# Optimization experiments

Hardware: AMD Instinct MI355X
Metric: run time of the kernel (lower is better)

Reference implementation:

```python
import jax, jax.numpy as jnp
import numpy as np

NUM_USR = 8192
H = 256  # NUM_SOURCE == H (feature dim of y_a); NUM_TARGET = 256


def setup_inputs() -> dict:
    key = jax.random.key(0)
    k1, k2, k3, k4 = jax.random.split(key, 4)
    return {
        "y_a": jax.random.normal(k1, (NUM_USR, H), dtype=jnp.float32),
        "y_b": jax.random.normal(k2, (NUM_USR, H), dtype=jnp.float32),
        "W": jax.random.normal(k3, (H, H), dtype=jnp.float32) * (1.0 / np.sqrt(H)),
        "b": jax.random.normal(k4, (H,), dtype=jnp.float32) * 0.01,
    }


def reference(y_a, y_b, W, b):
    # Linear: proj[j] = W @ y_b[j] + b   (torch nn.Linear convention)
    proj = jnp.einsum("jt,st->js", y_b, W) + b          # [num_usr, H]
    # torch loop computes score[i, j] = y_a[i] . proj[j], replicated H times
    # then averaged: out[i, k] = (1/H) * sum_j sigmoid(score[i, j])
    scores = jnp.einsum("ih,jh->ij", y_a, proj)          # [num_usr, num_usr]
    s = jnp.sum(jax.nn.sigmoid(scores), axis=1) / y_a.shape[1]  # [num_usr]
    return jnp.broadcast_to(s[:, None], y_a.shape)       # [num_usr, H]
```

## Files before the change

### kernel.cpp

```cpp
#include <hip/hip_runtime.h>

#define NUSR 8192
#define HDIM 256

typedef __attribute__((ext_vector_type(8))) __bf16 bf16x8;
typedef __attribute__((ext_vector_type(4))) float f32x4;

union frag_u { bf16x8 v; unsigned short u[8]; unsigned int d[4]; };

__device__ __forceinline__ unsigned int f2bf(float f) {
  unsigned u = __builtin_bit_cast(unsigned, f);
  u += 0x7FFFu + ((u >> 16) & 1u);
  return u >> 16;
}
__device__ __forceinline__ unsigned int f2bf2(float lo, float hi) {
  return f2bf(lo) | (f2bf(hi) << 16);
}
__device__ __forceinline__ float sigmoidf_fast(float x) {
  float e = __builtin_amdgcn_exp2f(x * -1.44269504088896340736f);
  return __builtin_amdgcn_rcpf(1.0f + e);
}


__global__ __launch_bounds__(256) void k1_fused(
    const float* __restrict__ ya, const float* __restrict__ yb,
    const float* __restrict__ W, const float* __restrict__ bvec,
    unsigned short* __restrict__ yabf, unsigned short* __restrict__ PX,
    float* __restrict__ svec)
{
  const int b   = blockIdx.x;
  const int tid = threadIdx.x;

  if (b < 256) {
    const int lane = tid & 63;
    const int w    = tid >> 6;
    const int q    = lane >> 4;
    const int i    = lane & 15;

    frag_u B[2][8];
#pragma unroll
    for (int g = 0; g < 2; ++g) {
      const float* ybrow = yb + (size_t)(b * 32 + g * 16 + i) * HDIM;
#pragma unroll
      for (int kb = 0; kb < 8; ++kb) {
        float4 v0 = *(const float4*)&ybrow[kb * 32 + q * 8];
        float4 v1 = *(const float4*)&ybrow[kb * 32 + q * 8 + 4];
        B[g][kb].d[0] = f2bf2(v0.x, v0.y); B[g][kb].d[1] = f2bf2(v0.z, v0.w);
        B[g][kb].d[2] = f2bf2(v1.x, v1.y); B[g][kb].d[3] = f2bf2(v1.z, v1.w);
      }
    }

#pragma unroll
    for (int t = 0; t < 4; ++t) {
      const int st = w * 4 + t;
      f32x4 acc[2] = {{0.f,0.f,0.f,0.f},{0.f,0.f,0.f,0.f}};
#pragma unroll
      for (int kb = 0; kb < 8; ++kb) {
        const float* wr = W + (size_t)(st * 16 + i) * HDIM + kb * 32 + q * 8;
        float4 w0 = *(const float4*)wr;
        float4 w1 = *(const float4*)(wr + 4);
        frag_u Af;
        Af.d[0] = f2bf2(w0.x, w0.y); Af.d[1] = f2bf2(w0.z, w0.w);
        Af.d[2] = f2bf2(w1.x, w1.y); Af.d[3] = f2bf2(w1.z, w1.w);
#pragma unroll
        for (int g = 0; g < 2; ++g)
          acc[g] = __builtin_amdgcn_mfma_f32_16x16x32_bf16(Af.v, B[g][kb].v, acc[g], 0, 0, 0);
      }
      float4 bias = *(const float4*)&bvec[st * 16 + q * 4];
#pragma unroll
      for (int g = 0; g < 2; ++g) {
        const int jg = b * 2 + g;
        unsigned v0 = f2bf2(acc[g][0] + bias.x, acc[g][1] + bias.y);
        unsigned v1 = f2bf2(acc[g][2] + bias.z, acc[g][3] + bias.w);
        size_t off = (size_t)jg * 4096 + (size_t)(st >> 1) * 512
                   + (size_t)(((st & 1) << 1) | (q >> 1)) * 128 + i * 8 + ((q & 1) * 4);
        *(uint2*)(PX + off) = make_uint2(v0, v1);
      }
    }
  } else {
    const int id = (b - 256) * 256 + tid;
    const float4* src = (const float4*)ya;
    uint4* dst = (uint4*)yabf;
#pragma unroll
    for (int u = 0; u < 4; ++u) {
      int d = id + u * 65536;
      float4 a = src[d * 2];
      float4 c = src[d * 2 + 1];
      uint4 o = { f2bf2(a.x, a.y), f2bf2(a.z, a.w),
                  f2bf2(c.x, c.y), f2bf2(c.z, c.w) };
      dst[d] = o;
    }
    if (b == 511) {
      float4 z = {0.f, 0.f, 0.f, 0.f};
      float4* sv = (float4*)svec;
#pragma unroll
      for (int u = 0; u < 8; ++u) sv[u * 256 + tid] = z;
    }
  }
}

__global__ __launch_bounds__(256, 2) void k2_score(
    const unsigned short* __restrict__ yabf, const unsigned short* __restrict__ PX,
    float* __restrict__ svec)
{
  __shared__ __align__(16) unsigned short bs[3][8192];
  const int tid  = threadIdx.x;
  const int lane = tid & 63;
  const int w    = tid >> 6;
  const int quad = lane >> 4;
  const int l15  = lane & 15;

  const int bid = blockIdx.x;
  const int xcd = bid & 7;
  const int k   = bid >> 3;
  const int by  = xcd * 2 + (k >> 5);
  const int bx  = k & 31;

  const int rbase = bx * 256 + w * 64;
  const int cg16  = by * 32;

  frag_u A[4][8];
#pragma unroll
  for (int g = 0; g < 4; ++g) {
    const unsigned short* src = yabf + (size_t)(rbase + g * 16 + l15) * HDIM;
#pragma unroll
    for (int kb = 0; kb < 8; ++kb)
      A[g][kb].v = *(const bf16x8*)&src[kb * 32 + quad * 8];
  }

  const unsigned short* psrc = PX + (size_t)cg16 * 4096;

  float rs[4][4] = {{0.f,0.f,0.f,0.f},{0.f,0.f,0.f,0.f},
                    {0.f,0.f,0.f,0.f},{0.f,0.f,0.f,0.f}};

#define STAGE(B, T)                                                          \
  do {                                                                       \
    const unsigned short* _src = psrc + (size_t)(T) * 8192;                  \
    unsigned short* _dst = &bs[(B)][0];                                      \
    _Pragma("unroll")                                                        \
    for (int p = 0; p < 4; ++p) {                                            \
      int c = p * 256 + tid;                                                 \
      __builtin_amdgcn_global_load_lds(                                      \
          (const __attribute__((address_space(1))) unsigned int*)(const void*)(_src + c * 8), \
          (__attribute__((address_space(3))) unsigned int*)(void*)(_dst + c * 8), \
          16, 0, 0);                                                         \
    }                                                                        \
  } while (0)

  STAGE(0, 0);
  STAGE(1, 1);

  int cb = 0, sb = 2;
  for (int t = 0; t < 16; ++t) {
    if (t < 15)
      asm volatile("s_waitcnt vmcnt(4)" ::: "memory");
    else
      asm volatile("s_waitcnt vmcnt(0)" ::: "memory");
    asm volatile("s_barrier" ::: "memory");
    if (t < 14)
      STAGE(sb, t + 2);

    const unsigned short* buf = &bs[cb][0];
#pragma unroll
    for (int tt = 0; tt < 2; ++tt) {
      f32x4 acc[4] = {{0.f,0.f,0.f,0.f},{0.f,0.f,0.f,0.f},
                      {0.f,0.f,0.f,0.f},{0.f,0.f,0.f,0.f}};
      __builtin_amdgcn_s_setprio(1);
#pragma unroll
      for (int kb = 0; kb < 8; ++kb) {
        bf16x8 bfrag = *(const bf16x8*)&buf[(tt * 512 + kb * 64 + lane) * 8];
#pragma unroll
        for (int g = 0; g < 4; ++g)
          acc[g] = __builtin_amdgcn_mfma_f32_16x16x32_bf16(A[g][kb].v, bfrag, acc[g], 0, 0, 0);
      }
      __builtin_amdgcn_s_setprio(0);
#pragma unroll
      for (int g = 0; g < 4; ++g)
#pragma unroll
        for (int r = 0; r < 4; ++r)
          rs[g][r] += sigmoidf_fast(acc[g][r]);
    }
    cb = (cb == 2) ? 0 : cb + 1;
    sb = (sb == 2) ? 0 : sb + 1;
  }
#undef STAGE

#pragma unroll
  for (int off = 1; off < 16; off <<= 1)
#pragma unroll
    for (int g = 0; g < 4; ++g)
#pragma unroll
      for (int r = 0; r < 4; ++r)
        rs[g][r] += __shfl_xor(rs[g][r], off, 64);

  if (l15 == 0) {
#pragma unroll
    for (int g = 0; g < 4; ++g)
#pragma unroll
      for (int r = 0; r < 4; ++r)
        atomicAdd(&svec[rbase + g * 16 + quad * 4 + r], rs[g][r]);
  }
}

__global__ __launch_bounds__(256) void k3_bcast(
    const float* __restrict__ svec, float* __restrict__ out)
{
  int idx = blockIdx.x * 256 + threadIdx.x;
  int row = idx >> 6;
  float v = svec[row] * (1.0f / 256.0f);
  float4 o = {v, v, v, v};
  ((float4*)out)[idx] = o;
}

extern "C" void kernel_launch(void* const* d_in, const int* in_sizes, int n_in,
                              void* d_out, int out_size, void* d_ws, size_t ws_size,
                              hipStream_t stream) {
  (void)in_sizes; (void)n_in; (void)out_size;
  const float* ya = (const float*)d_in[0];
  const float* yb = (const float*)d_in[1];
  const float* W  = (const float*)d_in[2];
  const float* bv = (const float*)d_in[3];
  float* out = (float*)d_out;

  char* ws = (char*)d_ws;
  unsigned short *PX, *yabf;
  float* svec;
  const size_t need = (8ull << 20) + (32ull << 10);
  if (ws_size >= need) {
    PX   = (unsigned short*)ws;
    yabf = (unsigned short*)(ws + (4 << 20));
    svec = (float*)(ws + (8 << 20));
  } else {
    PX   = (unsigned short*)d_out;
    yabf = (unsigned short*)((char*)d_out + (4 << 20));
    svec = (float*)ws;
  }

  k1_fused<<<512, 256, 0, stream>>>(ya, yb, W, bv, yabf, PX, svec);
  k2_score<<<512, 256, 0, stream>>>(yabf, PX, svec);
  k3_bcast<<<2048, 256, 0, stream>>>(svec, out);
}
```

Measured before the change: 122.6 us.

## Double-buffer larger LDS tiles and interleave sigmoid with MFMA phases in score kernel

Replaces the three-stage 16 KB LDS ring with two 32 KB buffers, each holding four 16-column tiles, so the loop runs 8 iterations instead of 16 and needs fewer barriers. The first PX tile load is now issued before the A-fragment register loads, so the two overlap. Within an iteration, two accumulator sets alternate so that each tile's sigmoid accumulation is interleaved with the next tile's MFMA phase, hiding transcendental latency behind matrix work. The cost is a full vmcnt(0) wait each iteration with only one tile in flight, more LDS per block, and a second accumulator set that raises register pressure and may lower occupancy.

```diff
diff --git a/kernel.cpp b/kernel.cpp
--- a/kernel.cpp
+++ b/kernel.cpp
@@ -103,7 +103,7 @@
     const unsigned short* __restrict__ yabf, const unsigned short* __restrict__ PX,
     float* __restrict__ svec)
 {
-  __shared__ __align__(16) unsigned short bs[3][8192];
+  __shared__ __align__(16) unsigned short bs[2][16384];
   const int tid  = threadIdx.x;
   const int lane = tid & 63;
   const int w    = tid >> 6;
@@ -119,26 +119,14 @@
   const int rbase = bx * 256 + w * 64;
   const int cg16  = by * 32;
 
-  frag_u A[4][8];
-#pragma unroll
-  for (int g = 0; g < 4; ++g) {
-    const unsigned short* src = yabf + (size_t)(rbase + g * 16 + l15) * HDIM;
-#pragma unroll
-    for (int kb = 0; kb < 8; ++kb)
-      A[g][kb].v = *(const bf16x8*)&src[kb * 32 + quad * 8];
-  }
-
   const unsigned short* psrc = PX + (size_t)cg16 * 4096;
-
-  float rs[4][4] = {{0.f,0.f,0.f,0.f},{0.f,0.f,0.f,0.f},
-                    {0.f,0.f,0.f,0.f},{0.f,0.f,0.f,0.f}};
 
 #define STAGE(B, T)                                                          \
   do {                                                                       \
-    const unsigned short* _src = psrc + (size_t)(T) * 8192;                  \
+    const unsigned short* _src = psrc + (size_t)(T) * 16384;                 \
     unsigned short* _dst = &bs[(B)][0];                                      \
     _Pragma("unroll")                                                        \
-    for (int p = 0; p < 4; ++p) {                                            \
+    for (int p = 0; p < 8; ++p) {                                            \
       int c = p * 256 + tid;                                                 \
       __builtin_amdgcn_global_load_lds(                                      \
           (const __attribute__((address_space(1))) unsigned int*)(const void*)(_src + c * 8), \
@@ -148,42 +136,64 @@
   } while (0)
 
   STAGE(0, 0);
-  STAGE(1, 1);
-
-  int cb = 0, sb = 2;
-  for (int t = 0; t < 16; ++t) {
-    if (t < 15)
-      asm volatile("s_waitcnt vmcnt(4)" ::: "memory");
-    else
-      asm volatile("s_waitcnt vmcnt(0)" ::: "memory");
+
+  frag_u A[4][8];
+#pragma unroll
+  for (int g = 0; g < 4; ++g) {
+    const unsigned short* src = yabf + (size_t)(rbase + g * 16 + l15) * HDIM;
+#pragma unroll
+    for (int kb = 0; kb < 8; ++kb)
+      A[g][kb].v = *(const bf16x8*)&src[kb * 32 + quad * 8];
+  }
+
+  float rs[4][4] = {{0.f,0.f,0.f,0.f},{0.f,0.f,0.f,0.f},
+                    {0.f,0.f,0.f,0.f},{0.f,0.f,0.f,0.f}};
+
+#define MFMA_PHASE(ACC, BUF, P)                                              \
+  do {                                                                       \
+    _Pragma("unroll")                                                        \
+    for (int g = 0; g < 4; ++g) ACC[g] = (f32x4){0.f, 0.f, 0.f, 0.f};        \
+    __builtin_amdgcn_s_setprio(1);                                           \
+    _Pragma("unroll")                                                        \
+    for (int kb = 0; kb < 8; ++kb) {                                         \
+      bf16x8 bfrag = *(const bf16x8*)&BUF[(P) * 4096 + kb * 512 + lane * 8]; \
+      _Pragma("unroll")                                                      \
+      for (int g = 0; g < 4; ++g)                                            \
+        ACC[g] = __builtin_amdgcn_mfma_f32_16x16x32_bf16(                    \
+            A[g][kb].v, bfrag, ACC[g], 0, 0, 0);                             \
+    }                                                                        \
+    __builtin_amdgcn_s_setprio(0);                                           \
+  } while (0)
+
+#define SIG(ACC)                                                             \
+  do {                                                                       \
+    _Pragma("unroll")                                                        \
+    for (int g = 0; g < 4; ++g)                                              \
+      _Pragma("unroll")                                                      \
+      for (int r = 0; r < 4; ++r)                                            \
+        rs[g][r] += sigmoidf_fast(ACC[g][r]);                                \
+  } while (0)
+
+  for (int t = 0; t < 8; ++t) {
+    asm volatile("s_waitcnt vmcnt(0)" ::: "memory");
     asm volatile("s_barrier" ::: "memory");
-    if (t < 14)
-      STAGE(sb, t + 2);
-
-    const unsigned short* buf = &bs[cb][0];
-#pragma unroll
-    for (int tt = 0; tt < 2; ++tt) {
-      f32x4 acc[4] = {{0.f,0.f,0.f,0.f},{0.f,0.f,0.f,0.f},
-                      {0.f,0.f,0.f,0.f},{0.f,0.f,0.f,0.f}};
-      __builtin_amdgcn_s_setprio(1);
-#pragma unroll
-      for (int kb = 0; kb < 8; ++kb) {
-        bf16x8 bfrag = *(const bf16x8*)&buf[(tt * 512 + kb * 64 + lane) * 8];
-#pragma unroll
-        for (int g = 0; g < 4; ++g)
-          acc[g] = __builtin_amdgcn_mfma_f32_16x16x32_bf16(A[g][kb].v, bfrag, acc[g], 0, 0, 0);
-      }
-      __builtin_amdgcn_s_setprio(0);
-#pragma unroll
-      for (int g = 0; g < 4; ++g)
-#pragma unroll
-        for (int r = 0; r < 4; ++r)
-          rs[g][r] += sigmoidf_fast(acc[g][r]);
-    }
-    cb = (cb == 2) ? 0 : cb + 1;
-    sb = (sb == 2) ? 0 : sb + 1;
+    if (t < 7)
+      STAGE((t + 1) & 1, t + 1);
+
+    const unsigned short* buf = &bs[t & 1][0];
+    f32x4 accA[4], accB[4];
+    MFMA_PHASE(accA, buf, 0);
+    MFMA_PHASE(accB, buf, 1);
+    SIG(accA);
+    MFMA_PHASE(accA, buf, 2);
+    SIG(accB);
+    MFMA_PHASE(accB, buf, 3);
+    SIG(accA);
+    SIG(accB);
   }
 #undef STAGE
+#undef MFMA_PHASE
+#undef SIG
 
 #pragma unroll
   for (int off = 1; off < 16; off <<= 1)
```

Result: no change. 122.3 us (-0.2%).
